# Optimization experiments

Hardware: AMD Instinct MI355X
Metric: run time of the kernel (lower is better)

## Reference

```python
import jax, jax.numpy as jnp
import numpy as np
from jax import lax

V = 32000   # vocab_size (len(word2id)+1)
I = 512     # txt_input_size (embedding dim / LSTM input)
H = 1024    # txt_hidden_size
IMG = 2048  # img_input_size == img_hidden_size (hidden_fc input)
B = 64      # batch
T = 64      # target length (decode runs T-1 steps)


def setup_inputs() -> dict:
    key = jax.random.key(0)
    ks = jax.random.split(key, 16)
    n = lambda k, shape, s=0.02: jax.random.normal(k, shape, jnp.float32) * s
    embed = n(ks[0], (V, I)).at[0].set(0.0)  # padding_idx=0 row is zero
    return {
        "src": jax.random.normal(ks[1], (B, IMG), jnp.float32),
        "tgt_ids": jax.random.randint(ks[2], (B, T), 0, V),
        "embed": embed,
        "W_h": n(ks[3], (H, IMG)), "b_h": jnp.zeros((H,), jnp.float32),
        "W_c": n(ks[4], (H, IMG)), "b_c": jnp.zeros((H,), jnp.float32),
        "W_ih": n(ks[5], (4 * H, I)), "W_hh": n(ks[6], (4 * H, H)),
        "b_ih": jnp.zeros((4 * H,), jnp.float32),
        "b_hh": jnp.zeros((4 * H,), jnp.float32),
        "W_out": n(ks[7], (V, H)), "b_out": jnp.zeros((V,), jnp.float32),
    }


def reference(src, tgt_ids, embed, W_h, b_h, W_c, b_c,
              W_ih, W_hh, b_ih, b_hh, W_out, b_out):
    # init_hidden: tanh(Linear(src)) for both hidden and cell
    h0 = jnp.tanh(src @ W_h.T + b_h)  # [B, H]
    c0 = jnp.tanh(src @ W_c.T + b_c)  # [B, H]

    x = embed[tgt_ids]                 # [B, T, I]
    xs = jnp.swapaxes(x[:, :-1, :], 0, 1)  # [T-1, B, I] teacher-forced inputs

    def step(carry, xt):
        h, c = carry
        g = xt @ W_ih.T + b_ih + h @ W_hh.T + b_hh  # [B, 4H], gate order i,f,g,o
        i, f, gg, o = jnp.split(g, 4, axis=-1)
        c = jax.nn.sigmoid(f) * c + jax.nn.sigmoid(i) * jnp.tanh(gg)
        h = jax.nn.sigmoid(o) * jnp.tanh(c)
        return (h, c), h

    _, hs = lax.scan(step, (h0, c0), xs)        # [T-1, B, H]
    outs = jnp.swapaxes(hs, 0, 1)               # [B, T-1, H]
    # dropout is identity in eval / deterministic reference
    logits = jnp.einsum('bth,vh->btv', outs, W_out) + b_out  # [B, T-1, V]
    logp = jax.nn.log_softmax(logits, axis=-1)

    tgt = tgt_ids[:, 1:]                        # [B, T-1]
    tok_lp = jnp.take_along_axis(logp, tgt[..., None], axis=2)[..., 0]
    mask = (tgt != 0)
    num_words = mask.sum()
    loss = -(tok_lp * mask).sum() / jnp.maximum(num_words, 1).astype(jnp.float32)
    return loss, num_words
```

## Files before the change

### kernel.cpp

```cpp
#include <hip/hip_runtime.h>
#include <math.h>

static constexpr int BB = 64;
static constexpr int TT = 64;
static constexpr int VV = 32000;
static constexpr int II = 512;
static constexpr int HH = 1024;
static constexpr int GG = 2048;
static constexpr int NT = 63;
static constexpr int NR = NT * BB;
static constexpr int MP = 4096;
static constexpr int NVB = 500;
static constexpr int VBS = 512;

using s16x8 = __attribute__((ext_vector_type(8))) short;
using f32x4 = __attribute__((ext_vector_type(4))) float;

__device__ __forceinline__ unsigned short f2bf(float f) {
    union { float f; unsigned u; } v; v.f = f;
    unsigned r = v.u + 0x7FFFu + ((v.u >> 16) & 1u);
    return (unsigned short)(r >> 16);
}
__device__ __forceinline__ float bf2f(unsigned short h) {
    union { unsigned u; float f; } v; v.u = ((unsigned)h) << 16;
    return v.f;
}

__device__ __forceinline__ void gload_lds16(const unsigned short* g,
                                            unsigned short* l) {
    __builtin_amdgcn_global_load_lds(
        (const __attribute__((address_space(1))) void*)g,
        (__attribute__((address_space(3))) void*)l, 16, 0, 0);
}

__global__ void cvt_kernel(const float* __restrict__ in,
                           unsigned short* __restrict__ out, int n4) {
    int idx = blockIdx.x * blockDim.x + threadIdx.x;
    int stride = gridDim.x * blockDim.x;
    for (int i = idx; i < n4; i += stride) {
        float4 v = ((const float4*)in)[i];
        ushort4 o;
        o.x = f2bf(v.x); o.y = f2bf(v.y); o.z = f2bf(v.z); o.w = f2bf(v.w);
        ((ushort4*)out)[i] = o;
    }
}

__global__ void gather_kernel(const float* __restrict__ embed,
                              const int* __restrict__ tgt_ids,
                              unsigned short* __restrict__ X,
                              int* __restrict__ TGT) {
    int idx = blockIdx.x * 256 + threadIdx.x;
    if (idx >= NR * (II / 4)) return;
    int r = idx / (II / 4);
    int kq = idx % (II / 4);
    int t = r / BB, b = r % BB;
    int tok = tgt_ids[b * TT + t];
    float4 v = ((const float4*)(embed + (size_t)tok * II))[kq];
    ushort4 o;
    o.x = f2bf(v.x); o.y = f2bf(v.y); o.z = f2bf(v.z); o.w = f2bf(v.w);
    ((ushort4*)(X + (size_t)r * II))[kq] = o;
    if (kq == 0) TGT[r] = tgt_ids[b * TT + t + 1];
}

__global__ __launch_bounds__(256) void init_hc_kernel(
    const float* __restrict__ src,
    const float* __restrict__ W_h, const float* __restrict__ b_h,
    const float* __restrict__ W_c, const float* __restrict__ b_c,
    unsigned short* __restrict__ HS, float* __restrict__ C) {
    int wave = blockIdx.x * 4 + (threadIdx.x >> 6);
    int lane = threadIdx.x & 63;
    int sel = wave >> 13;
    int rem = wave & 8191;
    int j = rem >> 3;
    int b0 = (rem & 7) * 8;
    const float* w = (sel ? W_c : W_h) + (size_t)j * GG;
    float acc[8] = {0.f,0.f,0.f,0.f,0.f,0.f,0.f,0.f};
    for (int k = lane; k < GG; k += 64) {
        float wv = w[k];
#pragma unroll
        for (int bb = 0; bb < 8; ++bb)
            acc[bb] += wv * src[(size_t)(b0 + bb) * GG + k];
    }
#pragma unroll
    for (int bb = 0; bb < 8; ++bb)
        for (int off = 32; off; off >>= 1)
            acc[bb] += __shfl_xor(acc[bb], off);
    if (lane == 0) {
        float bias = sel ? b_c[j] : b_h[j];
#pragma unroll
        for (int bb = 0; bb < 8; ++bb) {
            float v = tanhf(acc[bb] + bias);
            if (sel == 0) HS[(size_t)(b0 + bb) * HH + j] = f2bf(v);
            else          C[(size_t)(b0 + bb) * HH + j] = v;
        }
    }
}

template<int KTOT>
__device__ __forceinline__ void gemm_body(
    const unsigned short* __restrict__ Abase,
    const unsigned short* __restrict__ Bbase,
    unsigned short* Al, unsigned short* Bl,
    int tid, f32x4 (&acc)[4][4]) {
    int wv = tid >> 6, lane = tid & 63;
    int rl = lane & 15, ko0 = (lane >> 4) * 8;
    int wr = wv >> 1, wc = wv & 1;
    for (int kc = 0; kc < KTOT; kc += 64) {
        if (kc) __syncthreads();
#pragma unroll
        for (int it = 0; it < 4; ++it) {
            int c = it * 256 + tid;
            int row = c >> 3, k8 = (c & 7) * 8;
            unsigned short* ldsw = (unsigned short*)((it * 256 + wv * 64) * 8);
            gload_lds16(Abase + (size_t)row * KTOT + kc + k8,
                        Al + (size_t)(it * 256 + wv * 64) * 8);
            gload_lds16(Bbase + (size_t)row * KTOT + kc + k8,
                        Bl + (size_t)(it * 256 + wv * 64) * 8);
            (void)ldsw;
        }
        __syncthreads();
        const unsigned short* Ab = Al + (wr * 64 + rl) * 64 + ko0;
        const unsigned short* Bb = Bl + (wc * 64 + rl) * 64 + ko0;
#pragma unroll
        for (int ks = 0; ks < 2; ++ks) {
            s16x8 a[4], b[4];
#pragma unroll
            for (int mf = 0; mf < 4; ++mf)
                a[mf] = *(const s16x8*)(Ab + mf * 16 * 64 + ks * 32);
#pragma unroll
            for (int nf = 0; nf < 4; ++nf)
                b[nf] = *(const s16x8*)(Bb + nf * 16 * 64 + ks * 32);
#pragma unroll
            for (int mf = 0; mf < 4; ++mf)
#pragma unroll
                for (int nf = 0; nf < 4; ++nf)
                    acc[mf][nf] = __builtin_amdgcn_mfma_f32_16x16x32_bf16(
                        a[mf], b[nf], acc[mf][nf], 0, 0, 0);
        }
    }
}

__global__ __launch_bounds__(256) void gx_kernel(
    const unsigned short* __restrict__ X,
    const unsigned short* __restrict__ Wih,
    const float* __restrict__ b_ih, const float* __restrict__ b_hh,
    unsigned short* __restrict__ Gx) {
    __shared__ unsigned short Al[128 * 64];
    __shared__ unsigned short Bl[128 * 64];
    int tid = threadIdx.x;
    int mblk = blockIdx.x, nblk = blockIdx.y;
    int rbase = mblk * 128, v0 = nblk * 128;
    f32x4 acc[4][4];
#pragma unroll
    for (int mf = 0; mf < 4; ++mf)
#pragma unroll
        for (int nf = 0; nf < 4; ++nf) acc[mf][nf] = (f32x4){0.f,0.f,0.f,0.f};
    gemm_body<II>(X + (size_t)rbase * II, Wih + (size_t)v0 * II, Al, Bl, tid, acc);
    int wv = tid >> 6, lane = tid & 63;
    int rl = lane & 15, lg = lane >> 4;
    int wr = wv >> 1, wc = wv & 1;
    float bsum[4];
#pragma unroll
    for (int nf = 0; nf < 4; ++nf) {
        int col = v0 + wc * 64 + nf * 16 + rl;
        bsum[nf] = b_ih[col] + b_hh[col];
    }
#pragma unroll
    for (int mf = 0; mf < 4; ++mf)
#pragma unroll
        for (int q = 0; q < 4; ++q) {
            int r = rbase + wr * 64 + mf * 16 + lg * 4 + q;
#pragma unroll
            for (int nf = 0; nf < 4; ++nf) {
                int col = v0 + wc * 64 + nf * 16 + rl;
                Gx[(size_t)r * 4096 + col] = f2bf(acc[mf][nf][q] + bsum[nf]);
            }
        }
}

static constexpr int KP = 1032;
__global__ __launch_bounds__(256) void lstm_step_kernel(
    unsigned short* __restrict__ HS,
    const unsigned short* __restrict__ Gx,
    const unsigned short* __restrict__ Whh,
    float* __restrict__ C, int t) {
    __shared__ unsigned short Bs[16 * KP];
    __shared__ float R[64 * 16];
    int tid = threadIdx.x;
    int wv = tid >> 6, lane = tid & 63;
    int rl = lane & 15, lg = lane >> 4;
    int u0 = blockIdx.x * 4;
    const unsigned short* h = HS + (size_t)t * (BB * HH);
#pragma unroll
    for (int it = 0; it < 8; ++it) {
        int c = it * 256 + tid;
        int br = c >> 7, k8 = (c & 127) * 8;
        int wrow = (br >> 2) * HH + u0 + (br & 3);
        *(uint4*)&Bs[br * KP + k8] = *(const uint4*)(Whh + (size_t)wrow * HH + k8);
    }
    __syncthreads();
    const unsigned short* Ab = h + (size_t)(wv * 16 + rl) * HH;
    const unsigned short* Bb = Bs + rl * KP;
    f32x4 acc0 = {0.f,0.f,0.f,0.f}, acc1 = {0.f,0.f,0.f,0.f};
#pragma unroll
    for (int kc = 0; kc < HH; kc += 64) {
        int k0 = kc + lg * 8;
        s16x8 a0 = *(const s16x8*)(Ab + k0);
        s16x8 b0 = *(const s16x8*)(Bb + k0);
        acc0 = __builtin_amdgcn_mfma_f32_16x16x32_bf16(a0, b0, acc0, 0, 0, 0);
        s16x8 a1 = *(const s16x8*)(Ab + k0 + 32);
        s16x8 b1 = *(const s16x8*)(Bb + k0 + 32);
        acc1 = __builtin_amdgcn_mfma_f32_16x16x32_bf16(a1, b1, acc1, 0, 0, 0);
    }
    f32x4 acc = acc0 + acc1;
#pragma unroll
    for (int q = 0; q < 4; ++q) R[(wv * 16 + lg * 4 + q) * 16 + rl] = acc[q];
    __syncthreads();
    int row = tid >> 2, ul = tid & 3;
    int u = u0 + ul;
    const unsigned short* gx = Gx + (size_t)(t * BB + row) * 4096;
    float iv = R[row * 16 + 0 * 4 + ul] + bf2f(gx[0 * HH + u]);
    float fv = R[row * 16 + 1 * 4 + ul] + bf2f(gx[1 * HH + u]);
    float gv = R[row * 16 + 2 * 4 + ul] + bf2f(gx[2 * HH + u]);
    float ov = R[row * 16 + 3 * 4 + ul] + bf2f(gx[3 * HH + u]);
    float si = 1.f / (1.f + __expf(-iv));
    float sf = 1.f / (1.f + __expf(-fv));
    float so = 1.f / (1.f + __expf(-ov));
    float cold = C[(size_t)row * HH + u];
    float cnew = sf * cold + si * tanhf(gv);
    float hv = so * tanhf(cnew);
    C[(size_t)row * HH + u] = cnew;
    HS[(size_t)(t + 1) * (BB * HH) + (size_t)row * HH + u] = f2bf(hv);
}

__global__ __launch_bounds__(256) void logits_kernel(
    const unsigned short* __restrict__ A,
    const unsigned short* __restrict__ Wo,
    const float* __restrict__ b_out,
    const int* __restrict__ TGT,
    float* __restrict__ PM, float* __restrict__ PS,
    float* __restrict__ TLOG) {
    __shared__ unsigned short Al[128 * 64];
    __shared__ unsigned short Bl[128 * 64];
    int tid = threadIdx.x;
    int mblk = blockIdx.x, nblk = blockIdx.y;
    int rbase = mblk * 128, v0 = nblk * 128;
    f32x4 acc[4][4];
#pragma unroll
    for (int mf = 0; mf < 4; ++mf)
#pragma unroll
        for (int nf = 0; nf < 4; ++nf) acc[mf][nf] = (f32x4){0.f,0.f,0.f,0.f};
    gemm_body<HH>(A + (size_t)rbase * HH, Wo + (size_t)v0 * HH, Al, Bl, tid, acc);
    int wv = tid >> 6, lane = tid & 63;
    int rl = lane & 15, lg = lane >> 4;
    int wr = wv >> 1, wc = wv & 1;
    int cb = v0 + wc * 64;
    float bo[4];
#pragma unroll
    for (int nf = 0; nf < 4; ++nf) bo[nf] = b_out[cb + nf * 16 + rl];
    int vb = nblk * 2 + wc;
#pragma unroll
    for (int mf = 0; mf < 4; ++mf) {
        int rb = rbase + wr * 64 + mf * 16 + lg * 4;
#pragma unroll
        for (int q = 0; q < 4; ++q) {
            int r = rb + q;
            int tg = TGT[r];
            float e[4];
            float m = -1e30f;
#pragma unroll
            for (int nf = 0; nf < 4; ++nf) {
                e[nf] = acc[mf][nf][q] + bo[nf];
                if (cb + nf * 16 + rl == tg) TLOG[r] = e[nf];
                m = fmaxf(m, e[nf]);
            }
#pragma unroll
            for (int msk = 1; msk < 16; msk <<= 1) m = fmaxf(m, __shfl_xor(m, msk));
            float s = 0.f;
#pragma unroll
            for (int nf = 0; nf < 4; ++nf) s += __expf(e[nf] - m);
#pragma unroll
            for (int msk = 1; msk < 16; msk <<= 1) s += __shfl_xor(s, msk);
            if (rl == 0) {
                PM[(size_t)r * VBS + vb] = m;
                PS[(size_t)r * VBS + vb] = s;
            }
        }
    }
}

__global__ void rowred_kernel(const float* __restrict__ PM,
                              const float* __restrict__ PS,
                              const float* __restrict__ TLOG,
                              const int* __restrict__ TGT,
                              float* __restrict__ ROWLP) {
    int r = blockIdx.x * 4 + (threadIdx.x >> 6);
    int lane = threadIdx.x & 63;
    if (r >= NR) return;
    const float* pm = PM + (size_t)r * VBS;
    const float* ps = PS + (size_t)r * VBS;
    float m = -1e30f;
    for (int vb = lane; vb < NVB; vb += 64) m = fmaxf(m, pm[vb]);
    for (int off = 32; off; off >>= 1) m = fmaxf(m, __shfl_xor(m, off));
    float s = 0.f;
    for (int vb = lane; vb < NVB; vb += 64) s += ps[vb] * __expf(pm[vb] - m);
    for (int off = 32; off; off >>= 1) s += __shfl_xor(s, off);
    if (lane == 0) {
        float lse = m + logf(s);
        float lp = TLOG[r] - lse;
        ROWLP[r] = (TGT[r] != 0) ? lp : 0.f;
    }
}

__global__ void final_kernel(const float* __restrict__ ROWLP,
                             const int* __restrict__ TGT,
                             float* __restrict__ out) {
    int tid = threadIdx.x;
    float sum = 0.f; int cnt = 0;
    for (int r = tid; r < NR; r += 256) {
        sum += ROWLP[r];
        cnt += (TGT[r] != 0);
    }
    for (int off = 32; off; off >>= 1) {
        sum += __shfl_xor(sum, off);
        cnt += __shfl_xor(cnt, off);
    }
    __shared__ float wsum[4];
    __shared__ int wcnt[4];
    if ((tid & 63) == 0) { wsum[tid >> 6] = sum; wcnt[tid >> 6] = cnt; }
    __syncthreads();
    if (tid == 0) {
        float S = wsum[0] + wsum[1] + wsum[2] + wsum[3];
        int Cc = wcnt[0] + wcnt[1] + wcnt[2] + wcnt[3];
        out[0] = -S / fmaxf((float)Cc, 1.f);
        out[1] = (float)Cc;
    }
}

extern "C" void kernel_launch(void* const* d_in, const int* in_sizes, int n_in,
                              void* d_out, int out_size, void* d_ws, size_t ws_size,
                              hipStream_t stream) {
    const float* src    = (const float*)d_in[0];
    const int*   tgtids = (const int*)d_in[1];
    const float* embed  = (const float*)d_in[2];
    const float* W_h    = (const float*)d_in[3];
    const float* b_h    = (const float*)d_in[4];
    const float* W_c    = (const float*)d_in[5];
    const float* b_c    = (const float*)d_in[6];
    const float* W_ih   = (const float*)d_in[7];
    const float* W_hh   = (const float*)d_in[8];
    const float* b_ih   = (const float*)d_in[9];
    const float* b_hh   = (const float*)d_in[10];
    const float* W_out  = (const float*)d_in[11];
    const float* b_out  = (const float*)d_in[12];
    float* out = (float*)d_out;

    char* ws = (char*)d_ws;
    size_t off = 0;
    auto alloc = [&](size_t bytes) {
        size_t cur = off;
        off += (bytes + 255) & ~(size_t)255;
        return cur;
    };
    unsigned short* Wo_bf  = (unsigned short*)(ws + alloc((size_t)VV * HH * 2));
    unsigned short* Whh_bf = (unsigned short*)(ws + alloc((size_t)4 * HH * HH * 2));
    unsigned short* Wih_bf = (unsigned short*)(ws + alloc((size_t)4 * HH * II * 2));
    unsigned short* X_bf   = (unsigned short*)(ws + alloc((size_t)MP * II * 2));
    unsigned short* HS     = (unsigned short*)(ws + alloc((size_t)64 * BB * HH * 2));
    float* Cst   = (float*)(ws + alloc((size_t)BB * HH * 4));
    unsigned short* Gx = (unsigned short*)(ws + alloc((size_t)MP * 4096 * 2));
    float* PM    = (float*)(ws + alloc((size_t)MP * VBS * 4));
    float* PS    = (float*)(ws + alloc((size_t)MP * VBS * 4));
    float* TLOG  = (float*)(ws + alloc((size_t)MP * 4));
    int*   TGT   = (int*)(ws + alloc((size_t)MP * 4));
    float* ROWLP = (float*)(ws + alloc((size_t)NR * 4));

    cvt_kernel<<<4096, 256, 0, stream>>>(W_out, Wo_bf, VV * HH / 4);
    cvt_kernel<<<1024, 256, 0, stream>>>(W_hh, Whh_bf, 4 * HH * HH / 4);
    cvt_kernel<<<512, 256, 0, stream>>>(W_ih, Wih_bf, 4 * HH * II / 4);
    gather_kernel<<<(NR * (II / 4) + 255) / 256, 256, 0, stream>>>(embed, tgtids, X_bf, TGT);
    init_hc_kernel<<<4096, 256, 0, stream>>>(src, W_h, b_h, W_c, b_c, HS, Cst);
    gx_kernel<<<dim3(MP / 128, 4096 / 128), 256, 0, stream>>>(
        X_bf, Wih_bf, b_ih, b_hh, Gx);
    for (int t = 0; t < NT; ++t) {
        lstm_step_kernel<<<256, 256, 0, stream>>>(HS, Gx, Whh_bf, Cst, t);
    }
    logits_kernel<<<dim3(MP / 128, VV / 128), 256, 0, stream>>>(
        HS + (size_t)BB * HH, Wo_bf, b_out, TGT, PM, PS, TLOG);
    rowred_kernel<<<NR / 4, 256, 0, stream>>>(PM, PS, TLOG, TGT, ROWLP);
    final_kernel<<<1, 256, 0, stream>>>(ROWLP, TGT, out);
}
```

Before: 1.038 ms.

## Fuse LSTM steps into persistent cooperative kernel and swizzle GEMM LDS layout

Replaces the 63 per-timestep LSTM kernel launches with a single cooperative kernel of 64 blocks that keeps its W_hh slice resident in LDS and the cell state in registers, synchronizing timesteps with grid.sync. This removes repeated launch overhead and repeated reloading of W_hh from global memory each step. Separately, the shared GEMM body gains an XOR swizzle on the LDS layout to reduce bank conflicts. The trade-offs are grid-wide barrier cost and fewer, larger blocks, with only 64 CUs active during the recurrence.

```diff
diff --git a/kernel.cpp b/kernel.cpp
--- a/kernel.cpp
+++ b/kernel.cpp
@@ -1,5 +1,8 @@
 #include <hip/hip_runtime.h>
+#include <hip/hip_cooperative_groups.h>
 #include <math.h>
+
+namespace cg = cooperative_groups;
 
 static constexpr int BB = 64;
 static constexpr int TT = 64;
@@ -103,33 +106,32 @@
     unsigned short* Al, unsigned short* Bl,
     int tid, f32x4 (&acc)[4][4]) {
     int wv = tid >> 6, lane = tid & 63;
-    int rl = lane & 15, ko0 = (lane >> 4) * 8;
+    int rl = lane & 15, lg = lane >> 4;
     int wr = wv >> 1, wc = wv & 1;
+    int sw = rl & 7;
     for (int kc = 0; kc < KTOT; kc += 64) {
         if (kc) __syncthreads();
 #pragma unroll
         for (int it = 0; it < 4; ++it) {
             int c = it * 256 + tid;
-            int row = c >> 3, k8 = (c & 7) * 8;
-            unsigned short* ldsw = (unsigned short*)((it * 256 + wv * 64) * 8);
-            gload_lds16(Abase + (size_t)row * KTOT + kc + k8,
-                        Al + (size_t)(it * 256 + wv * 64) * 8);
-            gload_lds16(Bbase + (size_t)row * KTOT + kc + k8,
-                        Bl + (size_t)(it * 256 + wv * 64) * 8);
-            (void)ldsw;
+            int row = c >> 3, slot = c & 7;
+            int sslot = slot ^ (row & 7);
+            gload_lds16(Abase + (size_t)row * KTOT + kc + sslot * 8,
+                        Al + (size_t)c * 8);
+            gload_lds16(Bbase + (size_t)row * KTOT + kc + sslot * 8,
+                        Bl + (size_t)c * 8);
         }
         __syncthreads();
-        const unsigned short* Ab = Al + (wr * 64 + rl) * 64 + ko0;
-        const unsigned short* Bb = Bl + (wc * 64 + rl) * 64 + ko0;
 #pragma unroll
         for (int ks = 0; ks < 2; ++ks) {
+            int soff = ((ks * 4 + lg) ^ sw) * 8;
             s16x8 a[4], b[4];
 #pragma unroll
             for (int mf = 0; mf < 4; ++mf)
-                a[mf] = *(const s16x8*)(Ab + mf * 16 * 64 + ks * 32);
+                a[mf] = *(const s16x8*)&Al[(wr * 64 + mf * 16 + rl) * 64 + soff];
 #pragma unroll
             for (int nf = 0; nf < 4; ++nf)
-                b[nf] = *(const s16x8*)(Bb + nf * 16 * 64 + ks * 32);
+                b[nf] = *(const s16x8*)&Bl[(wc * 64 + nf * 16 + rl) * 64 + soff];
 #pragma unroll
             for (int mf = 0; mf < 4; ++mf)
 #pragma unroll
@@ -178,59 +180,66 @@
         }
 }
 
-static constexpr int KP = 1032;
-__global__ __launch_bounds__(256) void lstm_step_kernel(
+static constexpr int BSTR = 1032;
+__global__ __launch_bounds__(1024, 1) void lstm_scan_kernel(
     unsigned short* __restrict__ HS,
     const unsigned short* __restrict__ Gx,
     const unsigned short* __restrict__ Whh,
-    float* __restrict__ C, int t) {
-    __shared__ unsigned short Bs[16 * KP];
-    __shared__ float R[64 * 16];
+    const float* __restrict__ C0) {
+    __shared__ unsigned short Bs[64 * BSTR];
+    __shared__ float R[64 * 68];
     int tid = threadIdx.x;
-    int wv = tid >> 6, lane = tid & 63;
+    int u0 = blockIdx.x * 16;
+#pragma unroll
+    for (int it = 0; it < 8; ++it) {
+        int id = it * 1024 + tid;
+        int c = id >> 7, k8 = (id & 127) * 8;
+        int ul = c >> 2, g = c & 3;
+        *(uint4*)&Bs[c * BSTR + k8] =
+            *(const uint4*)(Whh + (size_t)(g * HH + u0 + ul) * HH + k8);
+    }
+    int grow = tid >> 4, gul = tid & 15;
+    float creg = C0[(size_t)grow * HH + u0 + gul];
+    int w = tid >> 6, lane = tid & 63;
+    int wr = w >> 2, wc = w & 3;
     int rl = lane & 15, lg = lane >> 4;
-    int u0 = blockIdx.x * 4;
-    const unsigned short* h = HS + (size_t)t * (BB * HH);
-#pragma unroll
-    for (int it = 0; it < 8; ++it) {
-        int c = it * 256 + tid;
-        int br = c >> 7, k8 = (c & 127) * 8;
-        int wrow = (br >> 2) * HH + u0 + (br & 3);
-        *(uint4*)&Bs[br * KP + k8] = *(const uint4*)(Whh + (size_t)wrow * HH + k8);
-    }
+    cg::grid_group grid = cg::this_grid();
     __syncthreads();
-    const unsigned short* Ab = h + (size_t)(wv * 16 + rl) * HH;
-    const unsigned short* Bb = Bs + rl * KP;
-    f32x4 acc0 = {0.f,0.f,0.f,0.f}, acc1 = {0.f,0.f,0.f,0.f};
-#pragma unroll
-    for (int kc = 0; kc < HH; kc += 64) {
-        int k0 = kc + lg * 8;
-        s16x8 a0 = *(const s16x8*)(Ab + k0);
-        s16x8 b0 = *(const s16x8*)(Bb + k0);
-        acc0 = __builtin_amdgcn_mfma_f32_16x16x32_bf16(a0, b0, acc0, 0, 0, 0);
-        s16x8 a1 = *(const s16x8*)(Ab + k0 + 32);
-        s16x8 b1 = *(const s16x8*)(Bb + k0 + 32);
-        acc1 = __builtin_amdgcn_mfma_f32_16x16x32_bf16(a1, b1, acc1, 0, 0, 0);
-    }
-    f32x4 acc = acc0 + acc1;
-#pragma unroll
-    for (int q = 0; q < 4; ++q) R[(wv * 16 + lg * 4 + q) * 16 + rl] = acc[q];
-    __syncthreads();
-    int row = tid >> 2, ul = tid & 3;
-    int u = u0 + ul;
-    const unsigned short* gx = Gx + (size_t)(t * BB + row) * 4096;
-    float iv = R[row * 16 + 0 * 4 + ul] + bf2f(gx[0 * HH + u]);
-    float fv = R[row * 16 + 1 * 4 + ul] + bf2f(gx[1 * HH + u]);
-    float gv = R[row * 16 + 2 * 4 + ul] + bf2f(gx[2 * HH + u]);
-    float ov = R[row * 16 + 3 * 4 + ul] + bf2f(gx[3 * HH + u]);
-    float si = 1.f / (1.f + __expf(-iv));
-    float sf = 1.f / (1.f + __expf(-fv));
-    float so = 1.f / (1.f + __expf(-ov));
-    float cold = C[(size_t)row * HH + u];
-    float cnew = sf * cold + si * tanhf(gv);
-    float hv = so * tanhf(cnew);
-    C[(size_t)row * HH + u] = cnew;
-    HS[(size_t)(t + 1) * (BB * HH) + (size_t)row * HH + u] = f2bf(hv);
+    for (int t = 0; t < NT; ++t) {
+        const unsigned short* Ab =
+            HS + (size_t)t * (BB * HH) + (size_t)(wr * 16 + rl) * HH + lg * 8;
+        const unsigned short* Bb = Bs + (wc * 16 + rl) * BSTR + lg * 8;
+        f32x4 acc0 = {0.f,0.f,0.f,0.f}, acc1 = {0.f,0.f,0.f,0.f};
+#pragma unroll
+        for (int kc = 0; kc < HH; kc += 64) {
+            s16x8 a0 = *(const s16x8*)(Ab + kc);
+            s16x8 b0 = *(const s16x8*)(Bb + kc);
+            acc0 = __builtin_amdgcn_mfma_f32_16x16x32_bf16(a0, b0, acc0, 0, 0, 0);
+            s16x8 a1 = *(const s16x8*)(Ab + kc + 32);
+            s16x8 b1 = *(const s16x8*)(Bb + kc + 32);
+            acc1 = __builtin_amdgcn_mfma_f32_16x16x32_bf16(a1, b1, acc1, 0, 0, 0);
+        }
+        f32x4 acc = acc0 + acc1;
+#pragma unroll
+        for (int q = 0; q < 4; ++q)
+            R[(wr * 16 + lg * 4 + q) * 68 + wc * 16 + rl] = acc[q];
+        __syncthreads();
+        float4 gv = *(const float4*)&R[grow * 68 + gul * 4];
+        const unsigned short* gx =
+            Gx + (size_t)(t * BB + grow) * 4096 + u0 + gul;
+        float iv = gv.x + bf2f(gx[0 * HH]);
+        float fv = gv.y + bf2f(gx[1 * HH]);
+        float gg = gv.z + bf2f(gx[2 * HH]);
+        float ov = gv.w + bf2f(gx[3 * HH]);
+        float si = 1.f / (1.f + __expf(-iv));
+        float sf = 1.f / (1.f + __expf(-fv));
+        float so = 1.f / (1.f + __expf(-ov));
+        creg = sf * creg + si * tanhf(gg);
+        float hv = so * tanhf(creg);
+        HS[(size_t)(t + 1) * (BB * HH) + (size_t)grow * HH + u0 + gul] = f2bf(hv);
+        __threadfence();
+        grid.sync();
+    }
 }
 
 __global__ __launch_bounds__(256) void logits_kernel(
@@ -366,7 +375,7 @@
     unsigned short* Whh_bf = (unsigned short*)(ws + alloc((size_t)4 * HH * HH * 2));
     unsigned short* Wih_bf = (unsigned short*)(ws + alloc((size_t)4 * HH * II * 2));
     unsigned short* X_bf   = (unsigned short*)(ws + alloc((size_t)MP * II * 2));
-    unsigned short* HS     = (unsigned short*)(ws + alloc((size_t)64 * BB * HH * 2));
+    unsigned short* HS     = (unsigned short*)(ws + alloc((size_t)65 * BB * HH * 2));
     float* Cst   = (float*)(ws + alloc((size_t)BB * HH * 4));
     unsigned short* Gx = (unsigned short*)(ws + alloc((size_t)MP * 4096 * 2));
     float* PM    = (float*)(ws + alloc((size_t)MP * VBS * 4));
@@ -382,8 +391,14 @@
     init_hc_kernel<<<4096, 256, 0, stream>>>(src, W_h, b_h, W_c, b_c, HS, Cst);
     gx_kernel<<<dim3(MP / 128, 4096 / 128), 256, 0, stream>>>(
         X_bf, Wih_bf, b_ih, b_hh, Gx);
-    for (int t = 0; t < NT; ++t) {
-        lstm_step_kernel<<<256, 256, 0, stream>>>(HS, Gx, Whh_bf, Cst, t);
+    {
+        unsigned short* hs_p = HS;
+        const unsigned short* gx_p = Gx;
+        const unsigned short* whh_p = Whh_bf;
+        const float* c0_p = Cst;
+        void* args[] = {&hs_p, &gx_p, &whh_p, &c0_p};
+        hipLaunchCooperativeKernel((void*)lstm_scan_kernel, dim3(64), dim3(1024),
+                                   args, 0, stream);
     }
     logits_kernel<<<dim3(MP / 128, VV / 128), 256, 0, stream>>>(
         HS + (size_t)BB * HH, Wo_bf, b_out, TGT, PM, PS, TLOG);
```

Result: slower. 3.192 ms (+207.5%).

## Swizzle GEMM LDS tiles and stream W_hh directly in LSTM step

Applied to the files above, without the earlier changes.

The shared GEMM body now stores A/B tiles in LDS with an XOR swizzle on the 16-byte slot index. This avoids bank conflicts when the MFMA fragments are read. The LSTM step kernel no longer stages its W_hh slice into shared memory and instead reads B fragments straight from global/L2, and it prefetches the Gx and cell-state values before the matmul to hide their latency. The HS buffer is enlarged by one timestep slot. This is a safety margin, though it risks more uncoalesced global traffic in the step kernel.

```diff
diff --git a/kernel.cpp b/kernel.cpp
--- a/kernel.cpp
+++ b/kernel.cpp
@@ -103,33 +103,32 @@
     unsigned short* Al, unsigned short* Bl,
     int tid, f32x4 (&acc)[4][4]) {
     int wv = tid >> 6, lane = tid & 63;
-    int rl = lane & 15, ko0 = (lane >> 4) * 8;
+    int rl = lane & 15, lg = lane >> 4;
     int wr = wv >> 1, wc = wv & 1;
+    int sw = rl & 7;
     for (int kc = 0; kc < KTOT; kc += 64) {
         if (kc) __syncthreads();
 #pragma unroll
         for (int it = 0; it < 4; ++it) {
             int c = it * 256 + tid;
-            int row = c >> 3, k8 = (c & 7) * 8;
-            unsigned short* ldsw = (unsigned short*)((it * 256 + wv * 64) * 8);
-            gload_lds16(Abase + (size_t)row * KTOT + kc + k8,
-                        Al + (size_t)(it * 256 + wv * 64) * 8);
-            gload_lds16(Bbase + (size_t)row * KTOT + kc + k8,
-                        Bl + (size_t)(it * 256 + wv * 64) * 8);
-            (void)ldsw;
+            int row = c >> 3, slot = c & 7;
+            int sslot = slot ^ (row & 7);
+            gload_lds16(Abase + (size_t)row * KTOT + kc + sslot * 8,
+                        Al + (size_t)c * 8);
+            gload_lds16(Bbase + (size_t)row * KTOT + kc + sslot * 8,
+                        Bl + (size_t)c * 8);
         }
         __syncthreads();
-        const unsigned short* Ab = Al + (wr * 64 + rl) * 64 + ko0;
-        const unsigned short* Bb = Bl + (wc * 64 + rl) * 64 + ko0;
 #pragma unroll
         for (int ks = 0; ks < 2; ++ks) {
+            int soff = ((ks * 4 + lg) ^ sw) * 8;
             s16x8 a[4], b[4];
 #pragma unroll
             for (int mf = 0; mf < 4; ++mf)
-                a[mf] = *(const s16x8*)(Ab + mf * 16 * 64 + ks * 32);
+                a[mf] = *(const s16x8*)&Al[(wr * 64 + mf * 16 + rl) * 64 + soff];
 #pragma unroll
             for (int nf = 0; nf < 4; ++nf)
-                b[nf] = *(const s16x8*)(Bb + nf * 16 * 64 + ks * 32);
+                b[nf] = *(const s16x8*)&Bl[(wc * 64 + nf * 16 + rl) * 64 + soff];
 #pragma unroll
             for (int mf = 0; mf < 4; ++mf)
 #pragma unroll
@@ -178,59 +177,51 @@
         }
 }
 
-static constexpr int KP = 1032;
 __global__ __launch_bounds__(256) void lstm_step_kernel(
     unsigned short* __restrict__ HS,
     const unsigned short* __restrict__ Gx,
     const unsigned short* __restrict__ Whh,
     float* __restrict__ C, int t) {
-    __shared__ unsigned short Bs[16 * KP];
     __shared__ float R[64 * 16];
     int tid = threadIdx.x;
     int wv = tid >> 6, lane = tid & 63;
     int rl = lane & 15, lg = lane >> 4;
     int u0 = blockIdx.x * 4;
+    int grow = tid >> 2, gul = tid & 3;
+    int gu = u0 + gul;
+    const unsigned short* gx = Gx + (size_t)(t * BB + grow) * 4096 + gu;
+    unsigned short gx0 = gx[0 * HH], gx1 = gx[1 * HH];
+    unsigned short gx2 = gx[2 * HH], gx3 = gx[3 * HH];
+    float cold = C[(size_t)grow * HH + gu];
     const unsigned short* h = HS + (size_t)t * (BB * HH);
-#pragma unroll
-    for (int it = 0; it < 8; ++it) {
-        int c = it * 256 + tid;
-        int br = c >> 7, k8 = (c & 127) * 8;
-        int wrow = (br >> 2) * HH + u0 + (br & 3);
-        *(uint4*)&Bs[br * KP + k8] = *(const uint4*)(Whh + (size_t)wrow * HH + k8);
-    }
-    __syncthreads();
-    const unsigned short* Ab = h + (size_t)(wv * 16 + rl) * HH;
-    const unsigned short* Bb = Bs + rl * KP;
+    const unsigned short* Ab = h + (size_t)(wv * 16 + rl) * HH + lg * 8;
+    int gate = rl >> 2, ul = rl & 3;
+    const unsigned short* Bb = Whh + (size_t)(gate * HH + u0 + ul) * HH + lg * 8;
     f32x4 acc0 = {0.f,0.f,0.f,0.f}, acc1 = {0.f,0.f,0.f,0.f};
 #pragma unroll
     for (int kc = 0; kc < HH; kc += 64) {
-        int k0 = kc + lg * 8;
-        s16x8 a0 = *(const s16x8*)(Ab + k0);
-        s16x8 b0 = *(const s16x8*)(Bb + k0);
+        s16x8 a0 = *(const s16x8*)(Ab + kc);
+        s16x8 b0 = *(const s16x8*)(Bb + kc);
         acc0 = __builtin_amdgcn_mfma_f32_16x16x32_bf16(a0, b0, acc0, 0, 0, 0);
-        s16x8 a1 = *(const s16x8*)(Ab + k0 + 32);
-        s16x8 b1 = *(const s16x8*)(Bb + k0 + 32);
+        s16x8 a1 = *(const s16x8*)(Ab + kc + 32);
+        s16x8 b1 = *(const s16x8*)(Bb + kc + 32);
         acc1 = __builtin_amdgcn_mfma_f32_16x16x32_bf16(a1, b1, acc1, 0, 0, 0);
     }
     f32x4 acc = acc0 + acc1;
 #pragma unroll
     for (int q = 0; q < 4; ++q) R[(wv * 16 + lg * 4 + q) * 16 + rl] = acc[q];
     __syncthreads();
-    int row = tid >> 2, ul = tid & 3;
-    int u = u0 + ul;
-    const unsigned short* gx = Gx + (size_t)(t * BB + row) * 4096;
-    float iv = R[row * 16 + 0 * 4 + ul] + bf2f(gx[0 * HH + u]);
-    float fv = R[row * 16 + 1 * 4 + ul] + bf2f(gx[1 * HH + u]);
-    float gv = R[row * 16 + 2 * 4 + ul] + bf2f(gx[2 * HH + u]);
-    float ov = R[row * 16 + 3 * 4 + ul] + bf2f(gx[3 * HH + u]);
+    float iv = R[grow * 16 + 0 * 4 + gul] + bf2f(gx0);
+    float fv = R[grow * 16 + 1 * 4 + gul] + bf2f(gx1);
+    float gv = R[grow * 16 + 2 * 4 + gul] + bf2f(gx2);
+    float ov = R[grow * 16 + 3 * 4 + gul] + bf2f(gx3);
     float si = 1.f / (1.f + __expf(-iv));
     float sf = 1.f / (1.f + __expf(-fv));
     float so = 1.f / (1.f + __expf(-ov));
-    float cold = C[(size_t)row * HH + u];
     float cnew = sf * cold + si * tanhf(gv);
     float hv = so * tanhf(cnew);
-    C[(size_t)row * HH + u] = cnew;
-    HS[(size_t)(t + 1) * (BB * HH) + (size_t)row * HH + u] = f2bf(hv);
+    C[(size_t)grow * HH + gu] = cnew;
+    HS[(size_t)(t + 1) * (BB * HH) + (size_t)grow * HH + gu] = f2bf(hv);
 }
 
 __global__ __launch_bounds__(256) void logits_kernel(
@@ -366,7 +357,7 @@
     unsigned short* Whh_bf = (unsigned short*)(ws + alloc((size_t)4 * HH * HH * 2));
     unsigned short* Wih_bf = (unsigned short*)(ws + alloc((size_t)4 * HH * II * 2));
     unsigned short* X_bf   = (unsigned short*)(ws + alloc((size_t)MP * II * 2));
-    unsigned short* HS     = (unsigned short*)(ws + alloc((size_t)64 * BB * HH * 2));
+    unsigned short* HS     = (unsigned short*)(ws + alloc((size_t)65 * BB * HH * 2));
     float* Cst   = (float*)(ws + alloc((size_t)BB * HH * 4));
     unsigned short* Gx = (unsigned short*)(ws + alloc((size_t)MP * 4096 * 2));
     float* PM    = (float*)(ws + alloc((size_t)MP * VBS * 4));
```

Measured after the change: 1.087 ms. 4.7% more time.
